# Optimization experiments

Hardware: AMD Instinct MI355X
Metric: run time of the kernel (lower is better)

## Reference

```python
import jax, jax.numpy as jnp
import numpy as np

N = 50000      # nodes
E = 800000     # edges
F_IN = 10      # node_feat_dim
H = 64         # hidden
ED = 3         # edge_dim
L = 3          # num_layers
EPS_LN = 1e-5


def _layernorm(x, g, b):
    mu = jnp.mean(x, axis=-1, keepdims=True)
    var = jnp.mean((x - mu) ** 2, axis=-1, keepdims=True)
    return (x - mu) * jax.lax.rsqrt(var + EPS_LN) * g + b


def setup_inputs() -> dict:
    key = jax.random.key(0)
    ks = jax.random.split(key, 20)
    x = jax.random.normal(ks[0], (N, F_IN), dtype=jnp.float32)
    edge_index = jax.random.randint(ks[1], (2, E), 0, N, dtype=jnp.int32)
    edge_attr = jax.random.uniform(ks[2], (E, ED), dtype=jnp.float32)

    def lin(k, fan_in, shape):
        return jax.random.normal(k, shape, dtype=jnp.float32) / np.sqrt(fan_in)

    params = {
        "Wp": lin(ks[3], F_IN, (F_IN, H)),
        "bp": jnp.zeros((H,), jnp.float32),
        # per-layer stacked params, leading dim L
        "ew1": lin(ks[4], ED, (L, ED, 16)),
        "eb1": jnp.zeros((L, 16), jnp.float32),
        "ew2": lin(ks[5], 16, (L, 16, 1)),
        "eb2": jnp.zeros((L, 1), jnp.float32),
        "nw": lin(ks[6], 2 * H, (L, 2 * H, H)),
        "nb": jnp.zeros((L, H), jnp.float32),
        "ln_g": jnp.ones((L, H), jnp.float32),
        "ln_b": jnp.zeros((L, H), jnp.float32),
        "hw1": lin(ks[7], H, (H, H // 2)),
        "hb1": jnp.zeros((H // 2,), jnp.float32),
        "hw2": lin(ks[8], H // 2, (H // 2, 1)),
        "hb2": jnp.zeros((1,), jnp.float32),
    }
    return {"x": x, "edge_index": edge_index, "edge_attr": edge_attr, **params}


def reference(x, edge_index, edge_attr, Wp, bp, ew1, eb1, ew2, eb2,
              nw, nb, ln_g, ln_b, hw1, hb1, hw2, hb2):
    src, dst = edge_index[0], edge_index[1]
    h = jax.nn.relu(x @ Wp + bp)                       # (N, H)
    for l in range(L):
        # edge MLP -> sigmoid weight per edge, shape (E, 1)
        ew = jax.nn.sigmoid(jax.nn.relu(edge_attr @ ew1[l] + eb1[l]) @ ew2[l] + eb2[l])
        msg = h[src] * ew                              # (E, H) gather + scale
        agg = jax.ops.segment_sum(msg, dst, num_segments=N)   # (N, H)
        cnt = jax.ops.segment_sum(ew, dst, num_segments=N)    # (N, 1)
        agg = agg / jnp.maximum(cnt, 1e-12)
        upd = jax.nn.relu(jnp.concatenate([h, agg], axis=1) @ nw[l] + nb[l])
        h = _layernorm(h + upd, ln_g[l], ln_b[l])
    return jax.nn.relu(h @ hw1 + hb1) @ hw2 + hb2      # (N, 1) logits
```

## Files before the change

kernel.cpp:

```cpp
#include <hip/hip_runtime.h>
#include <math.h>

#define N_NODES 50000
#define N_EDGES 800000
#define NPW 16
#define N_STRIPS 3125
#define N_BUCKETS 196
#define CAP_B 6144
#define CHUNK_A 2048
#define PROJ_BLOCKS 12500

typedef __attribute__((ext_vector_type(8))) short bf16x8;
typedef __attribute__((ext_vector_type(4))) float f32x4;
typedef __attribute__((ext_vector_type(2))) float f32x2;

__device__ __forceinline__ float bcast(float v, int lane) {
  return __int_as_float(__builtin_amdgcn_readlane(__float_as_int(v), lane));
}
__device__ __forceinline__ unsigned short f2bf(float f) {
  unsigned int u = __float_as_uint(f);
  u += 0x7FFFu + ((u >> 16) & 1u);
  return (unsigned short)(u >> 16);
}
__device__ __forceinline__ float bf2f(unsigned short s) {
  return __uint_as_float(((unsigned int)s) << 16);
}
__device__ __forceinline__ unsigned char f2fp8(float f) {
  return (unsigned char)(__builtin_amdgcn_cvt_pk_fp8_f32(f, f, 0, false) & 0xFF);
}

__global__ __launch_bounds__(256) void k_proj(const float* __restrict__ x,
                                              const float* __restrict__ Wp,
                                              const float* __restrict__ bp,
                                              unsigned short* __restrict__ hb,
                                              unsigned char* __restrict__ h8,
                                              int* __restrict__ bcur) {
  int bid = blockIdx.x;
  if (bid == PROJ_BLOCKS) {
    if (threadIdx.x < N_BUCKETS) bcur[threadIdx.x] = threadIdx.x * CAP_B;
    return;
  }
  int idx = bid * 256 + threadIdx.x;
  int n = idx >> 6, j = idx & 63;
  float acc = bp[j];
#pragma unroll
  for (int k = 0; k < 10; k++) acc += x[n * 10 + k] * Wp[k * 64 + j];
  float r = fmaxf(acc, 0.f);
  hb[n * 64 + j] = f2bf(r);
  h8[n * 64 + j] = f2fp8(r);
}

__global__ __launch_bounds__(256) void k_fillA(const int* __restrict__ ei,
                                               const float* __restrict__ ea,
                                               const float* __restrict__ ew1,
                                               const float* __restrict__ eb1,
                                               const float* __restrict__ ew2,
                                               const float* __restrict__ eb2,
                                               int* __restrict__ bcur,
                                               uint2* __restrict__ buf1) {
  __shared__ int lcnt[N_BUCKETS];
  __shared__ int gb[N_BUCKETS];
  for (int i = threadIdx.x; i < N_BUCKETS; i += 256) lcnt[i] = 0;
  __syncthreads();
  int base = blockIdx.x * CHUNK_A;
  uint2 rec[CHUNK_A / 256];
  int bk[CHUNK_A / 256], rk[CHUNK_A / 256];
#pragma unroll
  for (int k = 0; k < CHUNK_A / 256; k++) {
    int e = base + k * 256 + threadIdx.x;
    bk[k] = -1;
    if (e < N_EDGES) {
      int s = ei[e];
      int d = ei[N_EDGES + e];
      float a0 = ea[e * 3 + 0], a1 = ea[e * 3 + 1], a2 = ea[e * 3 + 2];
      int q[3];
#pragma unroll
      for (int l = 0; l < 3; l++) {
        float z = eb2[l];
#pragma unroll
        for (int t = 0; t < 16; t++) {
          float hd = a0 * ew1[l * 48 + t] + a1 * ew1[l * 48 + 16 + t] +
                     a2 * ew1[l * 48 + 32 + t] + eb1[l * 16 + t];
          z += fmaxf(hd, 0.f) * ew2[l * 16 + t];
        }
        float w = 1.f / (1.f + __expf(-z));
        q[l] = __float2int_rn(w * 8191.f);
      }
      unsigned int dl = (unsigned int)(d & 255);
      rec[k].x = (unsigned int)s | ((unsigned int)q[0] << 17) | ((dl & 3u) << 30);
      rec[k].y = (unsigned int)q[1] | ((unsigned int)q[2] << 13) | ((dl >> 2) << 26);
      int b = d >> 8;
      bk[k] = b;
      rk[k] = atomicAdd(&lcnt[b], 1);
    }
  }
  __syncthreads();
  if (threadIdx.x < N_BUCKETS) {
    int c = lcnt[threadIdx.x];
    gb[threadIdx.x] = c ? atomicAdd(&bcur[threadIdx.x], c) : 0;
  }
  __syncthreads();
#pragma unroll
  for (int k = 0; k < CHUNK_A / 256; k++)
    if (bk[k] >= 0) buf1[gb[bk[k]] + rk[k]] = rec[k];
}

__global__ __launch_bounds__(256) void k_fillB(const uint2* __restrict__ buf1,
                                               const int* __restrict__ bcur,
                                               uint2* __restrict__ csr,
                                               int* __restrict__ aoffs,
                                               int* __restrict__ adeg) {
  __shared__ int lhist[256];
  __shared__ int lscan[256];
  int b = blockIdx.x;
  int t = threadIdx.x;
  int segbase = b * CAP_B;
  int cnt = bcur[b] - segbase;
  lhist[t] = 0;
  __syncthreads();
  for (int i = t; i < cnt; i += 256) {
    uint2 rec = buf1[segbase + i];
    int dl = (int)((rec.x >> 30) | (((rec.y >> 26) & 63u) << 2));
    atomicAdd(&lhist[dl], 1);
  }
  __syncthreads();
  int v = lhist[t];
  lscan[t] = v;
  __syncthreads();
#pragma unroll
  for (int off = 1; off < 256; off <<= 1) {
    int u = (t >= off) ? lscan[t - off] : 0;
    __syncthreads();
    lscan[t] += u;
    __syncthreads();
  }
  int excl = lscan[t] - v;
  int nid = b * 256 + t;
  if (nid < N_NODES) {
    aoffs[nid] = segbase + excl;
    adeg[nid] = v;
  }
  __syncthreads();
  lhist[t] = segbase + excl;
  __syncthreads();
  for (int i = t; i < cnt; i += 256) {
    uint2 rec = buf1[segbase + i];
    int dl = (int)((rec.x >> 30) | (((rec.y >> 26) & 63u) << 2));
    int pos = atomicAdd(&lhist[dl], 1);
    csr[pos] = rec;
  }
}

template <int LI>
__device__ __forceinline__ float decw(uint2 c) {
  unsigned int q = (LI == 0) ? ((c.x >> 17) & 0x1FFFu)
                 : (LI == 1) ? (c.y & 0x1FFFu)
                             : ((c.y >> 13) & 0x1FFFu);
  return (float)q * (1.f / 8191.f);
}

template <int LI>
__global__ __launch_bounds__(256, 8) void k_agg(const uint2* __restrict__ csr,
                                                const int* __restrict__ aoffs,
                                                const int* __restrict__ adeg,
                                                const unsigned char* __restrict__ h8in,
                                                unsigned short* __restrict__ ab) {
  int lane = threadIdx.x & 63;
  int sub = lane >> 3;
  int jj = lane & 7;
  int gw = (blockIdx.x * 256 + threadIdx.x) >> 6;
  int n = gw * 8 + sub;
  bool active = n < N_NODES;
  int start = active ? aoffs[n] : 0;
  int d = active ? adeg[n] : 0;
  const uint2* hrow = (const uint2*)h8in;
  float a0 = 0.f, a1 = 0.f, a2 = 0.f, a3 = 0.f;
  float a4 = 0.f, a5 = 0.f, a6 = 0.f, a7 = 0.f, ws = 0.f;
  int i = 0;
  for (; i + 4 <= d; i += 4) {
    uint2 c0 = csr[start + i + 0];
    uint2 c1 = csr[start + i + 1];
    uint2 c2 = csr[start + i + 2];
    uint2 c3 = csr[start + i + 3];
    uint2 g0 = hrow[(c0.x & 0x1FFFFu) * 8 + jj];
    uint2 g1 = hrow[(c1.x & 0x1FFFFu) * 8 + jj];
    uint2 g2 = hrow[(c2.x & 0x1FFFFu) * 8 + jj];
    uint2 g3 = hrow[(c3.x & 0x1FFFFu) * 8 + jj];
    float w0 = decw<LI>(c0), w1 = decw<LI>(c1), w2 = decw<LI>(c2), w3 = decw<LI>(c3);
#pragma unroll
    for (int k = 0; k < 4; k++) {
      uint2 g = (k == 0) ? g0 : (k == 1) ? g1 : (k == 2) ? g2 : g3;
      float w = (k == 0) ? w0 : (k == 1) ? w1 : (k == 2) ? w2 : w3;
      f32x2 p01 = __builtin_amdgcn_cvt_pk_f32_fp8(g.x, false);
      f32x2 p23 = __builtin_amdgcn_cvt_pk_f32_fp8(g.x, true);
      f32x2 p45 = __builtin_amdgcn_cvt_pk_f32_fp8(g.y, false);
      f32x2 p67 = __builtin_amdgcn_cvt_pk_f32_fp8(g.y, true);
      a0 += p01[0] * w; a1 += p01[1] * w;
      a2 += p23[0] * w; a3 += p23[1] * w;
      a4 += p45[0] * w; a5 += p45[1] * w;
      a6 += p67[0] * w; a7 += p67[1] * w;
    }
    ws += w0 + w1 + w2 + w3;
  }
  for (; i < d; ++i) {
    uint2 c = csr[start + i];
    uint2 g = hrow[(c.x & 0x1FFFFu) * 8 + jj];
    float w = decw<LI>(c);
    f32x2 p01 = __builtin_amdgcn_cvt_pk_f32_fp8(g.x, false);
    f32x2 p23 = __builtin_amdgcn_cvt_pk_f32_fp8(g.x, true);
    f32x2 p45 = __builtin_amdgcn_cvt_pk_f32_fp8(g.y, false);
    f32x2 p67 = __builtin_amdgcn_cvt_pk_f32_fp8(g.y, true);
    a0 += p01[0] * w; a1 += p01[1] * w;
    a2 += p23[0] * w; a3 += p23[1] * w;
    a4 += p45[0] * w; a5 += p45[1] * w;
    a6 += p67[0] * w; a7 += p67[1] * w;
    ws += w;
  }
  if (active) {
    float inv = 1.f / fmaxf(ws, 1e-12f);
    uint4 o;
    o.x = (unsigned int)f2bf(a0 * inv) | ((unsigned int)f2bf(a1 * inv) << 16);
    o.y = (unsigned int)f2bf(a2 * inv) | ((unsigned int)f2bf(a3 * inv) << 16);
    o.z = (unsigned int)f2bf(a4 * inv) | ((unsigned int)f2bf(a5 * inv) << 16);
    o.w = (unsigned int)f2bf(a6 * inv) | ((unsigned int)f2bf(a7 * inv) << 16);
    ((uint4*)ab)[n * 8 + jj] = o;
  }
}

__global__ __launch_bounds__(256) void k_mlp(const float* __restrict__ nw,
                                             const float* __restrict__ nb,
                                             const float* __restrict__ g,
                                             const float* __restrict__ b,
                                             const unsigned short* __restrict__ hb_in,
                                             const unsigned short* __restrict__ ab_in,
                                             unsigned short* __restrict__ hbout,
                                             unsigned char* __restrict__ h8out) {
  int lane = threadIdx.x & 63;
  int n16 = lane & 15;
  int q = lane >> 4;
  int wid = (blockIdx.x * 256 + threadIdx.x) >> 6;
  int nwaves = gridDim.x * 4;

  bf16x8 bfr[4][4];
#pragma unroll
  for (int t = 0; t < 4; t++)
#pragma unroll
    for (int kc = 0; kc < 4; kc++) {
      bf16x8 v;
#pragma unroll
      for (int jj = 0; jj < 8; jj++) {
        int k = kc * 32 + q * 8 + jj;
        v[jj] = (short)f2bf(nw[k * 64 + t * 16 + n16]);
      }
      bfr[t][kc] = v;
    }
  float nbv[4], gv[4], bv[4];
#pragma unroll
  for (int t = 0; t < 4; t++) {
    nbv[t] = nb[t * 16 + n16];
    gv[t] = g[t * 16 + n16];
    bv[t] = b[t * 16 + n16];
  }

  for (int s = wid; s < N_STRIPS; s += nwaves) {
    int n0 = s * 16;
    f32x4 acc[4] = {{0.f, 0.f, 0.f, 0.f}, {0.f, 0.f, 0.f, 0.f},
                    {0.f, 0.f, 0.f, 0.f}, {0.f, 0.f, 0.f, 0.f}};
#pragma unroll
    for (int kc = 0; kc < 4; kc++) {
      const unsigned short* base = (kc < 2) ? hb_in : ab_in;
      bf16x8 a = *(const bf16x8*)(base + (size_t)(n0 + n16) * 64 + (kc & 1) * 32 + q * 8);
#pragma unroll
      for (int t = 0; t < 4; t++)
        acc[t] = __builtin_amdgcn_mfma_f32_16x16x32_bf16(a, bfr[t][kc], acc[t], 0, 0, 0);
    }
    float r[4][4];
    float p[4], p2[4];
#pragma unroll
    for (int rg = 0; rg < 4; rg++) { p[rg] = 0.f; p2[rg] = 0.f; }
#pragma unroll
    for (int t = 0; t < 4; t++)
#pragma unroll
      for (int rg = 0; rg < 4; rg++) {
        int row = n0 + q * 4 + rg;
        float hv = bf2f(hb_in[row * 64 + t * 16 + n16]);
        float rr = hv + fmaxf(acc[t][rg] + nbv[t], 0.f);
        r[t][rg] = rr;
        p[rg] += rr;
        p2[rg] += rr * rr;
      }
#pragma unroll
    for (int rg = 0; rg < 4; rg++)
#pragma unroll
      for (int off = 1; off < 16; off <<= 1) {
        p[rg] += __shfl_xor(p[rg], off);
        p2[rg] += __shfl_xor(p2[rg], off);
      }
#pragma unroll
    for (int rg = 0; rg < 4; rg++) {
      float mu = p[rg] * (1.f / 64.f);
      float var = p2[rg] * (1.f / 64.f) - mu * mu;
      float rs = rsqrtf(fmaxf(var, 0.f) + 1e-5f);
      int row = n0 + q * 4 + rg;
#pragma unroll
      for (int t = 0; t < 4; t++) {
        float o = (r[t][rg] - mu) * rs * gv[t] + bv[t];
        hbout[row * 64 + t * 16 + n16] = f2bf(o);
        h8out[row * 64 + t * 16 + n16] = f2fp8(o);
      }
    }
  }
}

__global__ __launch_bounds__(256, 2) void k_head(const float* __restrict__ hw1,
                                                 const float* __restrict__ hb1,
                                                 const float* __restrict__ hw2,
                                                 const float* __restrict__ hb2,
                                                 const unsigned short* __restrict__ hin,
                                                 float* __restrict__ out) {
  int j = threadIdx.x & 63;
  int jj = j & 31;
  int gw = (blockIdx.x * 256 + threadIdx.x) >> 6;
  float w1[64];
#pragma unroll
  for (int k = 0; k < 64; k++) w1[k] = hw1[k * 32 + jj];
  float hb1j = hb1[jj];
  float hw2j = hw2[jj];
  float hb2v = hb2[0];
  int n0 = gw * NPW;
  for (int n = n0; n < n0 + NPW; ++n) {
    if (n >= N_NODES) break;
    float hv = bf2f(hin[n * 64 + j]);
    float acc = hb1j;
#pragma unroll
    for (int k = 0; k < 64; k++) acc += bcast(hv, k) * w1[k];
    float z = fmaxf(acc, 0.f) * hw2j;
    if (j >= 32) z = 0.f;
#pragma unroll
    for (int off = 32; off; off >>= 1) z += __shfl_xor(z, off);
    if (j == 0) out[n] = z + hb2v;
  }
}

static inline size_t align256(size_t x) { return (x + 255) & ~size_t(255); }

extern "C" void kernel_launch(void* const* d_in, const int* in_sizes, int n_in,
                              void* d_out, int out_size, void* d_ws, size_t ws_size,
                              hipStream_t stream) {
  const float* x   = (const float*)d_in[0];
  const int*   ei  = (const int*)d_in[1];
  const float* ea  = (const float*)d_in[2];
  const float* Wp  = (const float*)d_in[3];
  const float* bp  = (const float*)d_in[4];
  const float* ew1 = (const float*)d_in[5];
  const float* eb1 = (const float*)d_in[6];
  const float* ew2 = (const float*)d_in[7];
  const float* eb2 = (const float*)d_in[8];
  const float* nw  = (const float*)d_in[9];
  const float* nb  = (const float*)d_in[10];
  const float* lng = (const float*)d_in[11];
  const float* lnb = (const float*)d_in[12];
  const float* hw1 = (const float*)d_in[13];
  const float* hb1 = (const float*)d_in[14];
  const float* hw2 = (const float*)d_in[15];
  const float* hb2 = (const float*)d_in[16];
  float* out = (float*)d_out;

  char* ws = (char*)d_ws;
  size_t off = 0;
  unsigned short* hb0  = (unsigned short*)(ws + off); off = align256(off + (size_t)N_NODES * 64 * 2);
  unsigned short* hb1b = (unsigned short*)(ws + off); off = align256(off + (size_t)N_NODES * 64 * 2);
  unsigned short* ab   = (unsigned short*)(ws + off); off = align256(off + (size_t)N_NODES * 64 * 2);
  unsigned char* h8_0  = (unsigned char*)(ws + off); off = align256(off + (size_t)N_NODES * 64);
  unsigned char* h8_1  = (unsigned char*)(ws + off); off = align256(off + (size_t)N_NODES * 64);
  uint2* csr  = (uint2*)(ws + off); off = align256(off + (size_t)N_BUCKETS * CAP_B * 8);
  uint2* buf1 = (uint2*)(ws + off); off = align256(off + (size_t)N_BUCKETS * CAP_B * 8);
  int* aoffs  = (int*)(ws + off); off = align256(off + (size_t)N_NODES * 4);
  int* adeg   = (int*)(ws + off); off = align256(off + (size_t)N_NODES * 4);
  int* bcur   = (int*)(ws + off); off = align256(off + 1024);

  k_proj<<<PROJ_BLOCKS + 1, 256, 0, stream>>>(x, Wp, bp, hb0, h8_0, bcur);
  k_fillA<<<(N_EDGES + CHUNK_A - 1) / CHUNK_A, 256, 0, stream>>>(ei, ea, ew1, eb1, ew2, eb2, bcur, buf1);
  k_fillB<<<N_BUCKETS, 256, 0, stream>>>(buf1, bcur, csr, aoffs, adeg);

  const int aggGrid = (N_NODES + 31) / 32;
  const int mlpGrid = 392;
  const int headGrid = ((N_NODES + NPW - 1) / NPW + 3) / 4;

  k_agg<0><<<aggGrid, 256, 0, stream>>>(csr, aoffs, adeg, h8_0, ab);
  k_mlp<<<mlpGrid, 256, 0, stream>>>(nw + 0 * 8192, nb + 0 * 64, lng + 0 * 64, lnb + 0 * 64,
                                     hb0, ab, hb1b, h8_1);
  k_agg<1><<<aggGrid, 256, 0, stream>>>(csr, aoffs, adeg, h8_1, ab);
  k_mlp<<<mlpGrid, 256, 0, stream>>>(nw + 1 * 8192, nb + 1 * 64, lng + 1 * 64, lnb + 1 * 64,
                                     hb1b, ab, hb0, h8_0);
  k_agg<2><<<aggGrid, 256, 0, stream>>>(csr, aoffs, adeg, h8_0, ab);
  k_mlp<<<mlpGrid, 256, 0, stream>>>(nw + 2 * 8192, nb + 2 * 64, lng + 2 * 64, lnb + 2 * 64,
                                     hb0, ab, hb1b, h8_1);

  k_head<<<headGrid, 256, 0, stream>>>(hw1, hb1, hw2, hb2, hb1b, out);
}
```

Measured before the change: 240.3 us.

## Degree-sort aggregation nodes, fuse head into last MLP, get residual via MFMA

Adds a k_order pass that buckets nodes by in-degree class so each aggregation wave handles nodes of similar degree, reducing lane divergence in the edge loop. This costs an extra small kernel and an indirect node-index load. The output head is fused into the final k_mlp as an MFMA on the LDS-staged normalized tile, removing a separate kernel and its re-read of h. The residual h is now recovered from the already-loaded A fragments via an identity-matrix MFMA instead of a second global load.

Result: faster. 223.3 us (-7.1%).

```diff
diff --git a/kernel.cpp b/kernel.cpp
--- a/kernel.cpp
+++ b/kernel.cpp
@@ -3,7 +3,6 @@
 
 #define N_NODES 50000
 #define N_EDGES 800000
-#define NPW 16
 #define N_STRIPS 3125
 #define N_BUCKETS 196
 #define CAP_B 6144
@@ -14,9 +13,6 @@
 typedef __attribute__((ext_vector_type(4))) float f32x4;
 typedef __attribute__((ext_vector_type(2))) float f32x2;
 
-__device__ __forceinline__ float bcast(float v, int lane) {
-  return __int_as_float(__builtin_amdgcn_readlane(__float_as_int(v), lane));
-}
 __device__ __forceinline__ unsigned short f2bf(float f) {
   unsigned int u = __float_as_uint(f);
   u += 0x7FFFu + ((u >> 16) & 1u);
@@ -34,10 +30,13 @@
                                               const float* __restrict__ bp,
                                               unsigned short* __restrict__ hb,
                                               unsigned char* __restrict__ h8,
-                                              int* __restrict__ bcur) {
+                                              int* __restrict__ bcur,
+                                              int* __restrict__ ocnt,
+                                              int* __restrict__ ocur) {
   int bid = blockIdx.x;
   if (bid == PROJ_BLOCKS) {
     if (threadIdx.x < N_BUCKETS) bcur[threadIdx.x] = threadIdx.x * CAP_B;
+    if (threadIdx.x < 8) { ocnt[threadIdx.x] = 0; ocur[threadIdx.x] = 0; }
     return;
   }
   int idx = bid * 256 + threadIdx.x;
@@ -109,14 +108,17 @@
                                                const int* __restrict__ bcur,
                                                uint2* __restrict__ csr,
                                                int* __restrict__ aoffs,
-                                               int* __restrict__ adeg) {
+                                               int* __restrict__ adeg,
+                                               int* __restrict__ ocnt) {
   __shared__ int lhist[256];
   __shared__ int lscan[256];
+  __shared__ int lcls[8];
   int b = blockIdx.x;
   int t = threadIdx.x;
   int segbase = b * CAP_B;
   int cnt = bcur[b] - segbase;
   lhist[t] = 0;
+  if (t < 8) lcls[t] = 0;
   __syncthreads();
   for (int i = t; i < cnt; i += 256) {
     uint2 rec = buf1[segbase + i];
@@ -139,8 +141,10 @@
   if (nid < N_NODES) {
     aoffs[nid] = segbase + excl;
     adeg[nid] = v;
-  }
-  __syncthreads();
+    atomicAdd(&lcls[min(v >> 2, 7)], 1);
+  }
+  __syncthreads();
+  if (t < 8 && lcls[t]) atomicAdd(&ocnt[t], lcls[t]);
   lhist[t] = segbase + excl;
   __syncthreads();
   for (int i = t; i < cnt; i += 256) {
@@ -149,6 +153,33 @@
     int pos = atomicAdd(&lhist[dl], 1);
     csr[pos] = rec;
   }
+}
+
+__global__ __launch_bounds__(256) void k_order(const int* __restrict__ adeg,
+                                               const int* __restrict__ ocnt,
+                                               int* __restrict__ ocur,
+                                               int* __restrict__ order) {
+  __shared__ int lc[8], gb[8];
+  int t = threadIdx.x;
+  int nid = blockIdx.x * 256 + t;
+  if (t < 8) lc[t] = 0;
+  __syncthreads();
+  int cls = 0, rank = 0;
+  bool act = nid < N_NODES;
+  if (act) {
+    cls = min(adeg[nid] >> 2, 7);
+    rank = atomicAdd(&lc[cls], 1);
+  }
+  __syncthreads();
+  if (t < 8) {
+    int base = 0;
+#pragma unroll
+    for (int c = 0; c < 8; c++) base += (c < t) ? ocnt[c] : 0;
+    int c = lc[t];
+    gb[t] = base + (c ? atomicAdd(&ocur[t], c) : 0);
+  }
+  __syncthreads();
+  if (act) order[gb[cls] + rank] = nid;
 }
 
 template <int LI>
@@ -163,14 +194,16 @@
 __global__ __launch_bounds__(256, 8) void k_agg(const uint2* __restrict__ csr,
                                                 const int* __restrict__ aoffs,
                                                 const int* __restrict__ adeg,
+                                                const int* __restrict__ order,
                                                 const unsigned char* __restrict__ h8in,
                                                 unsigned short* __restrict__ ab) {
   int lane = threadIdx.x & 63;
   int sub = lane >> 3;
   int jj = lane & 7;
   int gw = (blockIdx.x * 256 + threadIdx.x) >> 6;
-  int n = gw * 8 + sub;
-  bool active = n < N_NODES;
+  int idx = gw * 8 + sub;
+  bool active = idx < N_NODES;
+  int n = active ? order[idx] : 0;
   int start = active ? aoffs[n] : 0;
   int d = active ? adeg[n] : 0;
   const uint2* hrow = (const uint2*)h8in;
@@ -227,6 +260,7 @@
   }
 }
 
+template <bool HEAD>
 __global__ __launch_bounds__(256) void k_mlp(const float* __restrict__ nw,
                                              const float* __restrict__ nb,
                                              const float* __restrict__ g,
@@ -234,10 +268,17 @@
                                              const unsigned short* __restrict__ hb_in,
                                              const unsigned short* __restrict__ ab_in,
                                              unsigned short* __restrict__ hbout,
-                                             unsigned char* __restrict__ h8out) {
+                                             unsigned char* __restrict__ h8out,
+                                             const float* __restrict__ hw1,
+                                             const float* __restrict__ hb1,
+                                             const float* __restrict__ hw2,
+                                             const float* __restrict__ hb2,
+                                             float* __restrict__ out) {
+  __shared__ unsigned short lh[4][16 * 72];
   int lane = threadIdx.x & 63;
   int n16 = lane & 15;
   int q = lane >> 4;
+  int wv = threadIdx.x >> 6;
   int wid = (blockIdx.x * 256 + threadIdx.x) >> 6;
   int nwaves = gridDim.x * 4;
 
@@ -254,6 +295,15 @@
       }
       bfr[t][kc] = v;
     }
+  bf16x8 eye[2];
+#pragma unroll
+  for (int p = 0; p < 2; p++) {
+    bf16x8 v;
+#pragma unroll
+    for (int jj = 0; jj < 8; jj++)
+      v[jj] = ((q * 8 + jj) == (n16 + 16 * p)) ? (short)0x3F80 : (short)0;
+    eye[p] = v;
+  }
   float nbv[4], gv[4], bv[4];
 #pragma unroll
   for (int t = 0; t < 4; t++) {
@@ -261,18 +311,45 @@
     gv[t] = g[t * 16 + n16];
     bv[t] = b[t * 16 + n16];
   }
+  bf16x8 hfr[2][2];
+  float hb1v[2], hw2v[2], hb2v = 0.f;
+  if (HEAD) {
+#pragma unroll
+    for (int kc = 0; kc < 2; kc++)
+#pragma unroll
+      for (int tl = 0; tl < 2; tl++) {
+        bf16x8 v;
+#pragma unroll
+        for (int jj = 0; jj < 8; jj++)
+          v[jj] = (short)f2bf(hw1[(kc * 32 + q * 8 + jj) * 32 + tl * 16 + n16]);
+        hfr[kc][tl] = v;
+      }
+#pragma unroll
+    for (int tl = 0; tl < 2; tl++) {
+      hb1v[tl] = hb1[tl * 16 + n16];
+      hw2v[tl] = hw2[tl * 16 + n16];
+    }
+    hb2v = hb2[0];
+  }
 
   for (int s = wid; s < N_STRIPS; s += nwaves) {
     int n0 = s * 16;
     f32x4 acc[4] = {{0.f, 0.f, 0.f, 0.f}, {0.f, 0.f, 0.f, 0.f},
                     {0.f, 0.f, 0.f, 0.f}, {0.f, 0.f, 0.f, 0.f}};
+    bf16x8 afr[4];
 #pragma unroll
     for (int kc = 0; kc < 4; kc++) {
       const unsigned short* base = (kc < 2) ? hb_in : ab_in;
-      bf16x8 a = *(const bf16x8*)(base + (size_t)(n0 + n16) * 64 + (kc & 1) * 32 + q * 8);
+      afr[kc] = *(const bf16x8*)(base + (size_t)(n0 + n16) * 64 + (kc & 1) * 32 + q * 8);
 #pragma unroll
       for (int t = 0; t < 4; t++)
-        acc[t] = __builtin_amdgcn_mfma_f32_16x16x32_bf16(a, bfr[t][kc], acc[t], 0, 0, 0);
+        acc[t] = __builtin_amdgcn_mfma_f32_16x16x32_bf16(afr[kc], bfr[t][kc], acc[t], 0, 0, 0);
+    }
+    f32x4 rres[4];
+#pragma unroll
+    for (int t = 0; t < 4; t++) {
+      f32x4 z = {0.f, 0.f, 0.f, 0.f};
+      rres[t] = __builtin_amdgcn_mfma_f32_16x16x32_bf16(afr[t >> 1], eye[t & 1], z, 0, 0, 0);
     }
     float r[4][4];
     float p[4], p2[4];
@@ -282,9 +359,7 @@
     for (int t = 0; t < 4; t++)
 #pragma unroll
       for (int rg = 0; rg < 4; rg++) {
-        int row = n0 + q * 4 + rg;
-        float hv = bf2f(hb_in[row * 64 + t * 16 + n16]);
-        float rr = hv + fmaxf(acc[t][rg] + nbv[t], 0.f);
+        float rr = rres[t][rg] + fmaxf(acc[t][rg] + nbv[t], 0.f);
         r[t][rg] = rr;
         p[rg] += rr;
         p2[rg] += rr * rr;
@@ -305,40 +380,31 @@
 #pragma unroll
       for (int t = 0; t < 4; t++) {
         float o = (r[t][rg] - mu) * rs * gv[t] + bv[t];
-        hbout[row * 64 + t * 16 + n16] = f2bf(o);
+        unsigned short ob = f2bf(o);
+        hbout[row * 64 + t * 16 + n16] = ob;
         h8out[row * 64 + t * 16 + n16] = f2fp8(o);
-      }
-    }
-  }
-}
-
-__global__ __launch_bounds__(256, 2) void k_head(const float* __restrict__ hw1,
-                                                 const float* __restrict__ hb1,
-                                                 const float* __restrict__ hw2,
-                                                 const float* __restrict__ hb2,
-                                                 const unsigned short* __restrict__ hin,
-                                                 float* __restrict__ out) {
-  int j = threadIdx.x & 63;
-  int jj = j & 31;
-  int gw = (blockIdx.x * 256 + threadIdx.x) >> 6;
-  float w1[64];
-#pragma unroll
-  for (int k = 0; k < 64; k++) w1[k] = hw1[k * 32 + jj];
-  float hb1j = hb1[jj];
-  float hw2j = hw2[jj];
-  float hb2v = hb2[0];
-  int n0 = gw * NPW;
-  for (int n = n0; n < n0 + NPW; ++n) {
-    if (n >= N_NODES) break;
-    float hv = bf2f(hin[n * 64 + j]);
-    float acc = hb1j;
-#pragma unroll
-    for (int k = 0; k < 64; k++) acc += bcast(hv, k) * w1[k];
-    float z = fmaxf(acc, 0.f) * hw2j;
-    if (j >= 32) z = 0.f;
-#pragma unroll
-    for (int off = 32; off; off >>= 1) z += __shfl_xor(z, off);
-    if (j == 0) out[n] = z + hb2v;
+        if (HEAD) lh[wv][(q * 4 + rg) * 72 + t * 16 + n16] = ob;
+      }
+    }
+    if (HEAD) {
+      asm volatile("s_waitcnt lgkmcnt(0)" ::: "memory");
+      f32x4 hacc[2] = {{0.f, 0.f, 0.f, 0.f}, {0.f, 0.f, 0.f, 0.f}};
+#pragma unroll
+      for (int kc = 0; kc < 2; kc++) {
+        bf16x8 ha = *(const bf16x8*)&lh[wv][n16 * 72 + kc * 32 + q * 8];
+#pragma unroll
+        for (int tl = 0; tl < 2; tl++)
+          hacc[tl] = __builtin_amdgcn_mfma_f32_16x16x32_bf16(ha, hfr[kc][tl], hacc[tl], 0, 0, 0);
+      }
+#pragma unroll
+      for (int rg = 0; rg < 4; rg++) {
+        float sres = fmaxf(hacc[0][rg] + hb1v[0], 0.f) * hw2v[0] +
+                     fmaxf(hacc[1][rg] + hb1v[1], 0.f) * hw2v[1];
+#pragma unroll
+        for (int off = 1; off < 16; off <<= 1) sres += __shfl_xor(sres, off);
+        if (n16 == 0) out[n0 + q * 4 + rg] = sres + hb2v;
+      }
+    }
   }
 }
 
@@ -377,25 +443,26 @@
   uint2* buf1 = (uint2*)(ws + off); off = align256(off + (size_t)N_BUCKETS * CAP_B * 8);
   int* aoffs  = (int*)(ws + off); off = align256(off + (size_t)N_NODES * 4);
   int* adeg   = (int*)(ws + off); off = align256(off + (size_t)N_NODES * 4);
+  int* order  = (int*)(ws + off); off = align256(off + (size_t)N_NODES * 4);
   int* bcur   = (int*)(ws + off); off = align256(off + 1024);
-
-  k_proj<<<PROJ_BLOCKS + 1, 256, 0, stream>>>(x, Wp, bp, hb0, h8_0, bcur);
+  int* ocnt   = (int*)(ws + off); off = align256(off + 256);
+  int* ocur   = (int*)(ws + off); off = align256(off + 256);
+
+  k_proj<<<PROJ_BLOCKS + 1, 256, 0, stream>>>(x, Wp, bp, hb0, h8_0, bcur, ocnt, ocur);
   k_fillA<<<(N_EDGES + CHUNK_A - 1) / CHUNK_A, 256, 0, stream>>>(ei, ea, ew1, eb1, ew2, eb2, bcur, buf1);
-  k_fillB<<<N_BUCKETS, 256, 0, stream>>>(buf1, bcur, csr, aoffs, adeg);
+  k_fillB<<<N_BUCKETS, 256, 0, stream>>>(buf1, bcur, csr, aoffs, adeg, ocnt);
+  k_order<<<N_BUCKETS, 256, 0, stream>>>(adeg, ocnt, ocur, order);
 
   const int aggGrid = (N_NODES + 31) / 32;
   const int mlpGrid = 392;
-  const int headGrid = ((N_NODES + NPW - 1) / NPW + 3) / 4;
-
-  k_agg<0><<<aggGrid, 256, 0, stream>>>(csr, aoffs, adeg, h8_0, ab);
-  k_mlp<<<mlpGrid, 256, 0, stream>>>(nw + 0 * 8192, nb + 0 * 64, lng + 0 * 64, lnb + 0 * 64,
-                                     hb0, ab, hb1b, h8_1);
-  k_agg<1><<<aggGrid, 256, 0, stream>>>(csr, aoffs, adeg, h8_1, ab);
-  k_mlp<<<mlpGrid, 256, 0, stream>>>(nw + 1 * 8192, nb + 1 * 64, lng + 1 * 64, lnb + 1 * 64,
-                                     hb1b, ab, hb0, h8_0);
-  k_agg<2><<<aggGrid, 256, 0, stream>>>(csr, aoffs, adeg, h8_0, ab);
-  k_mlp<<<mlpGrid, 256, 0, stream>>>(nw + 2 * 8192, nb + 2 * 64, lng + 2 * 64, lnb + 2 * 64,
-                                     hb0, ab, hb1b, h8_1);
-
-  k_head<<<headGrid, 256, 0, stream>>>(hw1, hb1, hw2, hb2, hb1b, out);
-}
+
+  k_agg<0><<<aggGrid, 256, 0, stream>>>(csr, aoffs, adeg, order, h8_0, ab);
+  k_mlp<false><<<mlpGrid, 256, 0, stream>>>(nw + 0 * 8192, nb + 0 * 64, lng + 0 * 64, lnb + 0 * 64,
+                                            hb0, ab, hb1b, h8_1, hw1, hb1, hw2, hb2, out);
+  k_agg<1><<<aggGrid, 256, 0, stream>>>(csr, aoffs, adeg, order, h8_1, ab);
+  k_mlp<false><<<mlpGrid, 256, 0, stream>>>(nw + 1 * 8192, nb + 1 * 64, lng + 1 * 64, lnb + 1 * 64,
+                                            hb1b, ab, hb0, h8_0, hw1, hb1, hw2, hb2, out);
+  k_agg<2><<<aggGrid, 256, 0, stream>>>(csr, aoffs, adeg, order, h8_0, ab);
+  k_mlp<true><<<mlpGrid, 256, 0, stream>>>(nw + 2 * 8192, nb + 2 * 64, lng + 2 * 64, lnb + 2 * 64,
+                                           hb0, ab, hb1b, h8_1, hw1, hb1, hw2, hb2, out);
+}
```
